# Performance work log

Hardware: AMD Instinct MI355X
Metric: run time of the kernel (lower is better)

Reference implementation:

```python
import jax, jax.numpy as jnp
import numpy as np

D_MODEL = 1024
MAX_SEQ = 512
MAX_GRAPH = 1000
N_DEPTH = 20
N_ROLE = 4
B, T = 64, 512
VOCAB = 32000
N_REL = 8


def _sinusoidal(n, d, base):
    pos = jnp.arange(n, dtype=jnp.float32)[:, None]
    div = jnp.exp(jnp.arange(0, d, 2, dtype=jnp.float32) * (-np.log(base) / d))
    tab = jnp.zeros((n, d), jnp.float32)
    tab = tab.at[:, 0::2].set(jnp.sin(pos * div))
    tab = tab.at[:, 1::2].set(jnp.cos(pos * div))
    return tab


def setup_inputs() -> dict:
    key = jax.random.key(0)
    k1, k2, k3, k4 = jax.random.split(key, 4)
    input_ids = jax.random.randint(k1, (B, T), 0, VOCAB, dtype=jnp.int32)
    rel_ids = jax.random.randint(k2, (B, T), 0, N_REL, dtype=jnp.int32)
    seq_table = _sinusoidal(MAX_SEQ, D_MODEL, 10000.0)
    chain_table = _sinusoidal(MAX_GRAPH, D_MODEL, 5000.0)
    depth_table = 0.02 * jax.random.normal(k3, (N_DEPTH, D_MODEL), jnp.float32)
    role_table = 0.02 * jax.random.normal(k4, (N_ROLE, D_MODEL), jnp.float32)
    return {
        "input_ids": input_ids,
        "rel_ids": rel_ids,
        "seq_table": seq_table,
        "chain_table": chain_table,
        "depth_table": depth_table,
        "role_table": role_table,
    }


def _graph_positions(input_ids, rel_ids):
    # Vectorized equivalent of the original per-batch sequential scan.
    # chain_pos increments on rel>0 steps and resets to 0 when rel==0
    # immediately follows a rel>0 step.
    inc = (rel_ids > 0).astype(jnp.int32)
    c = jnp.cumsum(inc, axis=1) - inc  # exclusive cumsum = count of rel>0 before t
    prev_rel = jnp.pad(rel_ids[:, :-1], ((0, 0), (1, 0)))  # rel at t-1 (0 at t=0)
    reset = (rel_ids == 0) & (prev_rel > 0)
    baseline = jax.lax.cummax(jnp.where(reset, c, 0), axis=1)  # c at latest reset
    chain_positions = c - baseline
    # _is_relation_token is always False in the source, so depth never increments.
    depths = jnp.zeros_like(input_ids)
    # role: 3 for special tokens {0..4}, else 2 if rel==0, else 0 (1 unreachable)
    roles = jnp.where(input_ids <= 4, 3, jnp.where(rel_ids == 0, 2, 0))
    return chain_positions, depths, roles


def reference(input_ids, rel_ids, seq_table, chain_table, depth_table, role_table):
    Bx, Tx = input_ids.shape
    chain_positions, depths, roles = _graph_positions(input_ids, rel_ids)
    seq_emb = seq_table[:Tx][None, :, :]              # [1,T,D] broadcasts over B
    chain_emb = chain_table[chain_positions]          # [B,T,D]
    depth_emb = depth_table[depths]                   # [B,T,D]
    role_emb = role_table[roles]                      # [B,T,D]
    return seq_emb + 0.5 * chain_emb + 0.3 * depth_emb + 0.2 * role_emb
```

## Files before the change

### kernel.cpp

```cpp
#include <hip/hip_runtime.h>

#define D_MODEL 1024
#define T_SEQ   512
#define B_BATCH 64
#define ROWS_PER_BLOCK 8

typedef float nt_f4 __attribute__((ext_vector_type(4)));

__global__ __launch_bounds__(64) void gpe_scan_kernel(
    const int* __restrict__ input_ids,
    const int* __restrict__ rel_ids,
    int* __restrict__ cp_role)
{
    const int b    = blockIdx.x;
    const int lane = threadIdx.x;
    const int base = b * T_SEQ + lane * 8;

    const int4 ra = *reinterpret_cast<const int4*>(rel_ids + base);
    const int4 rb = *reinterpret_cast<const int4*>(rel_ids + base + 4);
    const int4 ia = *reinterpret_cast<const int4*>(input_ids + base);
    const int4 ib = *reinterpret_cast<const int4*>(input_ids + base + 4);
    const int rel[8] = {ra.x, ra.y, ra.z, ra.w, rb.x, rb.y, rb.z, rb.w};
    const int id[8]  = {ia.x, ia.y, ia.z, ia.w, ib.x, ib.y, ib.z, ib.w};

    int cl[8];
    int run = 0;
#pragma unroll
    for (int j = 0; j < 8; ++j) { cl[j] = run; run += (rel[j] > 0) ? 1 : 0; }

    int incl = run;
#pragma unroll
    for (int off = 1; off < 64; off <<= 1) {
        const int n = __shfl_up(incl, off);
        if (lane >= off) incl += n;
    }
    const int excl = incl - run;

    int c[8];
#pragma unroll
    for (int j = 0; j < 8; ++j) c[j] = excl + cl[j];

    int prev0 = __shfl_up(rel[7], 1);
    if (lane == 0) prev0 = 0;

    int ml[8];
    int mrun = 0;
#pragma unroll
    for (int j = 0; j < 8; ++j) {
        const int prl  = (j == 0) ? prev0 : rel[j - 1];
        const int mask = (rel[j] == 0 && prl > 0) ? c[j] : 0;
        mrun = max(mrun, mask);
        ml[j] = mrun;
    }

    int minc = mrun;
#pragma unroll
    for (int off = 1; off < 64; off <<= 1) {
        const int n = __shfl_up(minc, off);
        if (lane >= off) minc = max(minc, n);
    }
    int mexcl = __shfl_up(minc, 1);
    if (lane == 0) mexcl = 0;

    int outp[8];
#pragma unroll
    for (int j = 0; j < 8; ++j) {
        const int m    = max(mexcl, ml[j]);
        const int cp   = c[j] - m;
        const int role = (id[j] <= 4) ? 3 : ((rel[j] == 0) ? 2 : 0);
        outp[j] = cp | (role << 16);
    }
    *reinterpret_cast<int4*>(cp_role + base)     = make_int4(outp[0], outp[1], outp[2], outp[3]);
    *reinterpret_cast<int4*>(cp_role + base + 4) = make_int4(outp[4], outp[5], outp[6], outp[7]);
}

__global__ __launch_bounds__(256) void gpe_emb_kernel(
    const float* __restrict__ seq_table,
    const float* __restrict__ chain_table,
    const float* __restrict__ depth_table,
    const float* __restrict__ role_table,
    const int* __restrict__ cp_role,
    float* __restrict__ out)
{
    const int d0   = threadIdx.x << 2;
    const int row0 = blockIdx.x * ROWS_PER_BLOCK;

    int pr[ROWS_PER_BLOCK];
#pragma unroll
    for (int k = 0; k < ROWS_PER_BLOCK; ++k) pr[k] = cp_role[row0 + k];

    float4 basev[4];
    {
        const float4 dep = *reinterpret_cast<const float4*>(depth_table + d0);
#pragma unroll
        for (int r = 0; r < 4; ++r) {
            const float4 rv = *reinterpret_cast<const float4*>(role_table + r * D_MODEL + d0);
            basev[r].x = 0.3f * dep.x + 0.2f * rv.x;
            basev[r].y = 0.3f * dep.y + 0.2f * rv.y;
            basev[r].z = 0.3f * dep.z + 0.2f * rv.z;
            basev[r].w = 0.3f * dep.w + 0.2f * rv.w;
        }
    }

#pragma unroll
    for (int k = 0; k < ROWS_PER_BLOCK; ++k) {
        const int row  = row0 + k;
        const int t    = row & (T_SEQ - 1);
        const int cp   = pr[k] & 0xffff;
        const int role = pr[k] >> 16;

        const float4 sv = *reinterpret_cast<const float4*>(seq_table   + t  * D_MODEL + d0);
        const float4 cv = *reinterpret_cast<const float4*>(chain_table + cp * D_MODEL + d0);
        const float4 bv = basev[role];

        nt_f4 ov;
        ov.x = sv.x + 0.5f * cv.x + bv.x;
        ov.y = sv.y + 0.5f * cv.y + bv.y;
        ov.z = sv.z + 0.5f * cv.z + bv.z;
        ov.w = sv.w + 0.5f * cv.w + bv.w;

        __builtin_nontemporal_store(ov, reinterpret_cast<nt_f4*>(out + row * D_MODEL + d0));
    }
}

extern "C" void kernel_launch(void* const* d_in, const int* in_sizes, int n_in,
                              void* d_out, int out_size, void* d_ws, size_t ws_size,
                              hipStream_t stream) {
    const int* input_ids = (const int*)d_in[0];
    const int* rel_ids   = (const int*)d_in[1];
    const float* seq_table   = (const float*)d_in[2];
    const float* chain_table = (const float*)d_in[3];
    const float* depth_table = (const float*)d_in[4];
    const float* role_table  = (const float*)d_in[5];
    float* out = (float*)d_out;

    int* cp_role = (int*)d_ws;

    gpe_scan_kernel<<<B_BATCH, 64, 0, stream>>>(input_ids, rel_ids, cp_role);

    const int n_rows = B_BATCH * T_SEQ;
    gpe_emb_kernel<<<n_rows / ROWS_PER_BLOCK, 256, 0, stream>>>(
        seq_table, chain_table, depth_table, role_table, cp_role, out);
}
```

Baseline: 174.6 us.

## Group blocks by sequence position across batches to reuse seq row

```diff
diff --git a/kernel.cpp b/kernel.cpp
--- a/kernel.cpp
+++ b/kernel.cpp
@@ -3,7 +3,7 @@
 #define D_MODEL 1024
 #define T_SEQ   512
 #define B_BATCH 64
-#define ROWS_PER_BLOCK 8
+#define BGROUP  16
 
 typedef float nt_f4 __attribute__((ext_vector_type(4)));
 
@@ -82,44 +82,52 @@
     const int* __restrict__ cp_role,
     float* __restrict__ out)
 {
-    const int d0   = threadIdx.x << 2;
-    const int row0 = blockIdx.x * ROWS_PER_BLOCK;
+    const int d0 = threadIdx.x << 2;
+    const int t  = blockIdx.x & (T_SEQ - 1);
+    const int b0 = (blockIdx.x >> 9) * BGROUP;
 
-    int pr[ROWS_PER_BLOCK];
+    int pr[BGROUP];
 #pragma unroll
-    for (int k = 0; k < ROWS_PER_BLOCK; ++k) pr[k] = cp_role[row0 + k];
+    for (int k = 0; k < BGROUP; ++k)
+        pr[k] = cp_role[(b0 + k) * T_SEQ + t];
 
-    float4 basev[4];
-    {
-        const float4 dep = *reinterpret_cast<const float4*>(depth_table + d0);
-#pragma unroll
-        for (int r = 0; r < 4; ++r) {
-            const float4 rv = *reinterpret_cast<const float4*>(role_table + r * D_MODEL + d0);
-            basev[r].x = 0.3f * dep.x + 0.2f * rv.x;
-            basev[r].y = 0.3f * dep.y + 0.2f * rv.y;
-            basev[r].z = 0.3f * dep.z + 0.2f * rv.z;
-            basev[r].w = 0.3f * dep.w + 0.2f * rv.w;
-        }
-    }
+    const float4 sv  = *reinterpret_cast<const float4*>(seq_table   + t * D_MODEL + d0);
+    const float4 dep = *reinterpret_cast<const float4*>(depth_table + d0);
+    const float4 rv0 = *reinterpret_cast<const float4*>(role_table  + 0 * D_MODEL + d0);
+    const float4 rv2 = *reinterpret_cast<const float4*>(role_table  + 2 * D_MODEL + d0);
+    const float4 rv3 = *reinterpret_cast<const float4*>(role_table  + 3 * D_MODEL + d0);
+
+    float4 sd;
+    sd.x = sv.x + 0.3f * dep.x;
+    sd.y = sv.y + 0.3f * dep.y;
+    sd.z = sv.z + 0.3f * dep.z;
+    sd.w = sv.w + 0.3f * dep.w;
+
+    float4 b0v, b2v, b3v;
+    b0v.x = sd.x + 0.2f * rv0.x;  b0v.y = sd.y + 0.2f * rv0.y;
+    b0v.z = sd.z + 0.2f * rv0.z;  b0v.w = sd.w + 0.2f * rv0.w;
+    b2v.x = sd.x + 0.2f * rv2.x;  b2v.y = sd.y + 0.2f * rv2.y;
+    b2v.z = sd.z + 0.2f * rv2.z;  b2v.w = sd.w + 0.2f * rv2.w;
+    b3v.x = sd.x + 0.2f * rv3.x;  b3v.y = sd.y + 0.2f * rv3.y;
+    b3v.z = sd.z + 0.2f * rv3.z;  b3v.w = sd.w + 0.2f * rv3.w;
 
 #pragma unroll
-    for (int k = 0; k < ROWS_PER_BLOCK; ++k) {
-        const int row  = row0 + k;
-        const int t    = row & (T_SEQ - 1);
+    for (int k = 0; k < BGROUP; ++k) {
         const int cp   = pr[k] & 0xffff;
         const int role = pr[k] >> 16;
 
-        const float4 sv = *reinterpret_cast<const float4*>(seq_table   + t  * D_MODEL + d0);
         const float4 cv = *reinterpret_cast<const float4*>(chain_table + cp * D_MODEL + d0);
-        const float4 bv = basev[role];
+
+        const float4 bv = (role == 3) ? b3v : ((role == 2) ? b2v : b0v);
 
         nt_f4 ov;
-        ov.x = sv.x + 0.5f * cv.x + bv.x;
-        ov.y = sv.y + 0.5f * cv.y + bv.y;
-        ov.z = sv.z + 0.5f * cv.z + bv.z;
-        ov.w = sv.w + 0.5f * cv.w + bv.w;
+        ov.x = bv.x + 0.5f * cv.x;
+        ov.y = bv.y + 0.5f * cv.y;
+        ov.z = bv.z + 0.5f * cv.z;
+        ov.w = bv.w + 0.5f * cv.w;
 
-        __builtin_nontemporal_store(ov, reinterpret_cast<nt_f4*>(out + row * D_MODEL + d0));
+        __builtin_nontemporal_store(
+            ov, reinterpret_cast<nt_f4*>(out + ((b0 + k) * T_SEQ + t) * D_MODEL + d0));
     }
 }
 
@@ -138,7 +146,7 @@
 
     gpe_scan_kernel<<<B_BATCH, 64, 0, stream>>>(input_ids, rel_ids, cp_role);
 
-    const int n_rows = B_BATCH * T_SEQ;
-    gpe_emb_kernel<<<n_rows / ROWS_PER_BLOCK, 256, 0, stream>>>(
+    const int n_blocks = (B_BATCH / BGROUP) * T_SEQ;
+    gpe_emb_kernel<<<n_blocks, 256, 0, stream>>>(
         seq_table, chain_table, depth_table, role_table, cp_role, out);
 }
```

Result: faster. 153.5 us (-12.1%).
